# Kernel optimization log

Measured on AMD Instinct MI355X. Metric: run time of the kernel, lower is better.

## Reference

```python
import jax, jax.numpy as jnp
import numpy as np

PATCHES = 196
HEADS = 12


def build_attention_mask(patches, memory_tokens_list, extension=False):
    """Additive mask: masked entries -inf, allowed entries 0. Shape (1, Sq, Skv)."""
    class_tokens = len(memory_tokens_list) + 1
    input_tokens = patches + class_tokens
    total_tokens = input_tokens + sum(memory_tokens_list)
    mask = np.zeros((1, input_tokens, total_tokens), dtype=np.float32)
    mask[:, :, patches + 1:] = -np.inf
    prev = 0
    for i, mtok in enumerate(memory_tokens_list):
        ct = patches + 1 + i
        ms = input_tokens + prev
        me = ms + mtok
        if extension:
            mask[:, ct:, ct] = 0.0
            mask[:, ct:, ms:me] = 0.0
        else:
            mask[:, ct, ct] = 0.0
            mask[:, ct, ms:me] = 0.0
        prev += mtok
    return mask


def setup_inputs() -> dict:
    key = jax.random.key(0)
    ks = jax.random.split(key, 5)
    B, Sq, D, M = 64, PATCHES + 2, 768, 8  # 1 base class token + 1 memory class token
    std = 0.02
    return {
        "hidden_states": jax.random.normal(ks[0], (B, Sq, D), jnp.float32),
        "memory": jax.random.normal(ks[1], (1, M, D), jnp.float32) * std,
        "Wq": jax.random.normal(ks[2], (D, D), jnp.float32) * std,
        "bq": jnp.zeros((D,), jnp.float32),
        "Wk": jax.random.normal(ks[3], (D, D), jnp.float32) * std,
        "bk": jnp.zeros((D,), jnp.float32),
        "Wv": jax.random.normal(ks[4], (D, D), jnp.float32) * std,
        "bv": jnp.zeros((D,), jnp.float32),
    }


def _split_heads(x, heads):
    B, S, D = x.shape
    return x.reshape(B, S, heads, D // heads)  # bshd


def reference(hidden_states, memory, Wq, bq, Wk, bk, Wv, bv):
    B, Sq, D = hidden_states.shape
    M = memory.shape[1]
    head_dim = D // HEADS
    scale = 1.0 / jnp.sqrt(jnp.asarray(head_dim, hidden_states.dtype))
    # static additive mask (1, Sq, Skv)
    mask = jnp.asarray(build_attention_mask(PATCHES, [M]))

    with_memory = jnp.concatenate(
        [hidden_states, jnp.broadcast_to(memory, (B, M, D))], axis=1)  # (B, Skv, D)

    q = _split_heads(hidden_states @ Wq + bq, HEADS)  # (B,Sq,H,dh)
    k = _split_heads(with_memory @ Wk + bk, HEADS)    # (B,Skv,H,dh)
    v = _split_heads(with_memory @ Wv + bv, HEADS)

    scores = jnp.einsum("bqhd,bkhd->bhqk", q, k) * scale + mask[:, None]  # (B,H,Sq,Skv)
    probs = jax.nn.softmax(scores, axis=-1)  # dropout is identity in eval
    ctx = jnp.einsum("bhqk,bkhd->bqhd", probs, v)
    return ctx.reshape(B, Sq, D)
```

## Files before the change

### kernel.cpp

```cpp
#include <hip/hip_runtime.h>

typedef __attribute__((ext_vector_type(8))) short bf16x8;
typedef __attribute__((ext_vector_type(4))) float f32x4;
typedef __attribute__((ext_vector_type(4))) unsigned int u32x4;

#define NB 64
#define SQ 198
#define SKV 206
#define DM 768
#define NH 12
#define NROWS (NB * SKV)
#define NCOL 2304

static __device__ __forceinline__ unsigned short f2b(float f) {
  union { float f; unsigned u; } v; v.f = f;
  unsigned r = v.u + 0x7FFFu + ((v.u >> 16) & 1u);
  return (unsigned short)(r >> 16);
}

typedef const __attribute__((address_space(1))) unsigned int g_u32;
typedef __attribute__((address_space(3))) unsigned int l_u32;
static __device__ __forceinline__ void gload_lds16(const void* g, void* l) {
  __builtin_amdgcn_global_load_lds((g_u32*)g, (l_u32*)l, 16, 0, 0);
}

__global__ __launch_bounds__(256) void k_conv_x(const float* __restrict__ hid,
                                                const float* __restrict__ mem,
                                                unsigned short* __restrict__ xkv) {
  int idx = (blockIdx.x * 256 + threadIdx.x) * 8;
  int r = idx / DM;
  int c = idx - r * DM;
  int b = r / SKV, s = r - b * SKV;
  const float* src = (s < SQ) ? (hid + (b * SQ + s) * DM + c)
                              : (mem + (s - SQ) * DM + c);
  float4 v0 = ((const float4*)src)[0];
  float4 v1 = ((const float4*)src)[1];
  unsigned w0 = f2b(v0.x) | ((unsigned)f2b(v0.y) << 16);
  unsigned w1 = f2b(v0.z) | ((unsigned)f2b(v0.w) << 16);
  unsigned w2 = f2b(v1.x) | ((unsigned)f2b(v1.y) << 16);
  unsigned w3 = f2b(v1.z) | ((unsigned)f2b(v1.w) << 16);
  u32x4 o = {w0, w1, w2, w3};
  *(u32x4*)(xkv + idx) = o;
}

__global__ __launch_bounds__(256) void k_conv_w(const float* __restrict__ Wq,
                                                const float* __restrict__ Wk,
                                                const float* __restrict__ Wv,
                                                unsigned short* __restrict__ wt) {
  __shared__ float L[64][65];
  int w = blockIdx.z;
  int n0 = blockIdx.x * 64, k0 = blockIdx.y * 64;
  const float* W = (w == 0) ? Wq : (w == 1) ? Wk : Wv;
  int tid = threadIdx.x;
#pragma unroll
  for (int i = 0; i < 16; ++i) {
    int idx = i * 256 + tid;
    int lr = idx >> 6, lc = idx & 63;
    L[lr][lc] = W[(k0 + lr) * DM + n0 + lc];
  }
  __syncthreads();
  unsigned short* dst = wt + w * DM * DM;
#pragma unroll
  for (int o = 0; o < 2; ++o) {
    int gi = o * 256 + tid;
    int rn = gi >> 3, g = gi & 7;
    unsigned wrd[4];
#pragma unroll
    for (int jj = 0; jj < 4; ++jj) {
      float f0 = L[g * 8 + jj * 2 + 0][rn];
      float f1 = L[g * 8 + jj * 2 + 1][rn];
      wrd[jj] = f2b(f0) | ((unsigned)f2b(f1) << 16);
    }
    u32x4 o4 = {wrd[0], wrd[1], wrd[2], wrd[3]};
    *(u32x4*)(dst + (n0 + rn) * DM + k0 + g * 8) = o4;
  }
}

__global__ __launch_bounds__(512, 2) void k_gemm(const unsigned short* __restrict__ xkv,
                                                 const unsigned short* __restrict__ wt,
                                                 const float* __restrict__ bq,
                                                 const float* __restrict__ bk,
                                                 const float* __restrict__ bv,
                                                 unsigned short* __restrict__ cout) {
  __shared__ __align__(16) unsigned char smem[131072];
  int o = blockIdx.x, xcd = o & 7, rest = o >> 3;
  int sid = (xcd < 4 ? xcd * 59 : 236 + (xcd - 4) * 58) + rest;
  int mtile = sid / 9, ntile = sid - mtile * 9;
  int row0 = mtile * 256, col0 = ntile * 256;
  int w = ntile / 3;
  int colw0 = (ntile - w * 3) * 256;
  int tid = threadIdx.x, lane = tid & 63, wid = tid >> 6;
  int wm = wid >> 2, wn = wid & 3;
  int l = lane & 15, gq = lane >> 4;
  const unsigned short* wbase = wt + w * DM * DM;

  int sr = tid >> 2, pg = tid & 3, sg = pg ^ (sr & 3);
  int arow0 = row0 + sr;        if (arow0 > NROWS - 1) arow0 = NROWS - 1;
  int arow1 = row0 + 128 + sr;  if (arow1 > NROWS - 1) arow1 = NROWS - 1;
  const unsigned short* aP0 = xkv + arow0 * DM + sg * 8;
  const unsigned short* aP1 = xkv + arow1 * DM + sg * 8;
  const unsigned short* bP0 = wbase + (colw0 + sr) * DM + sg * 8;
  const unsigned short* bP1 = wbase + (colw0 + 128 + sr) * DM + sg * 8;
  int ldsW = wid * 1024;

  f32x4 zero = {0.f, 0.f, 0.f, 0.f};
  f32x4 acc[8][4];
#pragma unroll
  for (int i = 0; i < 8; ++i)
#pragma unroll
    for (int j = 0; j < 4; ++j) acc[i][j] = zero;

#pragma unroll
  for (int p = 0; p < 3; ++p) {
    gload_lds16(aP0 + p * 32, smem + p * 16384 + ldsW);
    gload_lds16(aP1 + p * 32, smem + p * 16384 + 8192 + ldsW);
    gload_lds16(bP0 + p * 32, smem + 65536 + p * 16384 + ldsW);
    gload_lds16(bP1 + p * 32, smem + 65536 + p * 16384 + 8192 + ldsW);
  }

  int swx = (gq * 16) ^ ((l & 3) << 4);
  int aRd = (wm * 128 + l) * 64 + swx;
  int bRd = 65536 + (wn * 64 + l) * 64 + swx;

  auto doTile = [&](int t) {
    int bo = (t & 3) * 16384;
    bf16x8 a[8], b[4];
#pragma unroll
    for (int mi = 0; mi < 8; ++mi) a[mi] = *(const bf16x8*)(smem + bo + aRd + mi * 1024);
#pragma unroll
    for (int ni = 0; ni < 4; ++ni) b[ni] = *(const bf16x8*)(smem + bo + bRd + ni * 1024);
    __builtin_amdgcn_s_setprio(1);
#pragma unroll
    for (int mi = 0; mi < 8; ++mi)
#pragma unroll
      for (int ni = 0; ni < 4; ++ni)
        acc[mi][ni] = __builtin_amdgcn_mfma_f32_16x16x32_bf16(a[mi], b[ni], acc[mi][ni], 0, 0, 0);
    __builtin_amdgcn_s_setprio(0);
  };

#pragma unroll 1
  for (int t = 0; t < 22; ++t) {
    asm volatile("s_waitcnt vmcnt(8)" ::: "memory");
    __builtin_amdgcn_s_barrier();
    asm volatile("" ::: "memory");
    if (t < 21) {
      int io = ((t + 3) & 3) * 16384;
      int kI = (t + 3) * 32;
      gload_lds16(aP0 + kI, smem + io + ldsW);
      gload_lds16(aP1 + kI, smem + io + 8192 + ldsW);
      gload_lds16(bP0 + kI, smem + 65536 + io + ldsW);
      gload_lds16(bP1 + kI, smem + 65536 + io + 8192 + ldsW);
    }
    doTile(t);
  }
  asm volatile("s_waitcnt vmcnt(4)" ::: "memory");
  __builtin_amdgcn_s_barrier();
  asm volatile("" ::: "memory");
  doTile(22);
  asm volatile("s_waitcnt vmcnt(0)" ::: "memory");
  __builtin_amdgcn_s_barrier();
  asm volatile("" ::: "memory");
  doTile(23);

  const float* bias = (w == 0) ? bq : (w == 1) ? bk : bv;
  float bb[4];
#pragma unroll
  for (int ni = 0; ni < 4; ++ni) bb[ni] = bias[colw0 + wn * 64 + ni * 16 + l];

  __syncthreads();
#pragma unroll
  for (int mi = 0; mi < 8; ++mi)
#pragma unroll
    for (int ni = 0; ni < 4; ++ni)
#pragma unroll
      for (int rr = 0; rr < 4; ++rr) {
        int row = wm * 128 + mi * 16 + gq * 4 + rr;
        int col = wn * 64 + ni * 16 + l;
        *(unsigned short*)(smem + row * 512 + ((col * 2) ^ ((row & 7) << 4))) =
            f2b(acc[mi][ni][rr] + bb[ni]);
      }
  __syncthreads();
#pragma unroll
  for (int it = 0; it < 16; ++it) {
    int gi = it * 512 + tid;
    int row = gi >> 5, gran = gi & 31;
    if (row0 + row < NROWS) {
      u32x4 v = *(const u32x4*)(smem + row * 512 + ((gran * 16) ^ ((row & 7) << 4)));
      *(u32x4*)(cout + (row0 + row) * NCOL + col0 + gran * 8) = v;
    }
  }
}

static __device__ __forceinline__ int vt_off(int row, int col) {
  return row * 416 + ((col * 2) ^ (((row >> 3) & 1) << 4));
}

__global__ __launch_bounds__(256, 3) void k_attn(const unsigned short* __restrict__ cqkv,
                                                 float* __restrict__ out) {
  __shared__ __align__(16) unsigned short Ksh[208 * 64];
  __shared__ __align__(16) unsigned char  VtB[64 * 416];
  int bh = blockIdx.x;
  int b = bh / NH, h = bh - b * NH;
  int tid = threadIdx.x, lane = tid & 63, wid = tid >> 6;
  int g = lane >> 4, l = lane & 15;
  const unsigned short* Cb = cqkv + (b * SKV) * NCOL + h * 64;

  if (tid < 64) *(unsigned*)(VtB + vt_off(tid, 206)) = 0u;
  for (int i = tid; i < 208 * 8; i += 256) {
    int row = i >> 3, gg = i & 7;
    int srow = (row < SKV) ? row : (SKV - 1);
    u32x4 v = *(const u32x4*)(Cb + srow * NCOL + 768 + gg * 8);
    *(u32x4*)((unsigned char*)Ksh + ((row * 128 + gg * 16) ^ ((row & 7) << 4))) = v;
  }
  for (int i = tid; i < 206 * 8; i += 256) {
    int key = i >> 3, gg = i & 7;
    u32x4 v = *(const u32x4*)(Cb + key * NCOL + 1536 + gg * 8);
    union { u32x4 v4; unsigned short e[8]; } u; u.v4 = v;
#pragma unroll
    for (int j = 0; j < 8; ++j)
      *(unsigned short*)(VtB + vt_off(gg * 8 + j, key)) = u.e[j];
  }
  __syncthreads();

  const float scale = 0.125f;
  f32x4 zero4 = {0.f, 0.f, 0.f, 0.f};
  int srcA = ((g & 1) << 5) + l;
  int srcB = srcA + 16;
  bool hiHalf = (g >= 2);

  for (int qt = wid; qt < 13; qt += 4) {
    int qr = qt * 16 + l;
    int qld = qr > 197 ? 197 : qr;
    const unsigned short* qp = Cb + qld * NCOL + g * 8;
    bf16x8 qa0 = *(const bf16x8*)qp;
    bf16x8 qa1 = *(const bf16x8*)(qp + 32);

    f32x4 sc[13];
#pragma unroll
    for (int nt = 0; nt < 13; ++nt) sc[nt] = zero4;
#pragma unroll
    for (int nt = 0; nt < 13; ++nt) {
      int key = nt * 16 + l;
      int rb = key * 128, sw = (key & 7) << 4, kb = g * 16;
      bf16x8 kb0 = *(const bf16x8*)((const unsigned char*)Ksh + rb + (kb ^ sw));
      bf16x8 kb1 = *(const bf16x8*)((const unsigned char*)Ksh + rb + ((kb + 64) ^ sw));
      sc[nt] = __builtin_amdgcn_mfma_f32_16x16x32_bf16(kb0, qa0, sc[nt], 0, 0, 0);
      sc[nt] = __builtin_amdgcn_mfma_f32_16x16x32_bf16(kb1, qa1, sc[nt], 0, 0, 0);
    }

    float mx = -1e30f;
#pragma unroll
    for (int nt = 0; nt < 13; ++nt)
#pragma unroll
      for (int r = 0; r < 4; ++r) {
        int key = nt * 16 + g * 4 + r;
        float s = sc[nt][r] * scale;
        bool ok = (key < 197 || qr == 197) && (key < SKV);
        s = ok ? s : -1e30f;
        sc[nt][r] = s;
        mx = fmaxf(mx, s);
      }
    mx = fmaxf(mx, __shfl_xor(mx, 16));
    mx = fmaxf(mx, __shfl_xor(mx, 32));
    float sum = 0.f;
#pragma unroll
    for (int nt = 0; nt < 13; ++nt)
#pragma unroll
      for (int r = 0; r < 4; ++r) {
        float p = __expf(sc[nt][r] - mx);
        sc[nt][r] = p;
        sum += p;
      }
    sum += __shfl_xor(sum, 16);
    sum += __shfl_xor(sum, 32);
    float inv = 1.0f / sum;

    unsigned pk0[13], pk1[13];
#pragma unroll
    for (int nt = 0; nt < 13; ++nt) {
      asm("v_cvt_pk_bf16_f32 %0, %1, %2" : "=v"(pk0[nt]) : "v"(sc[nt][0]), "v"(sc[nt][1]));
      asm("v_cvt_pk_bf16_f32 %0, %1, %2" : "=v"(pk1[nt]) : "v"(sc[nt][2]), "v"(sc[nt][3]));
    }

    f32x4 ctx[4];
#pragma unroll
    for (int dt = 0; dt < 4; ++dt) ctx[dt] = zero4;
#pragma unroll
    for (int c = 0; c < 7; ++c) {
      union { unsigned w[4]; bf16x8 v; } pa;
      if (c < 6) {
        int n0 = 2 * c, n1 = 2 * c + 1;
        unsigned a0 = (unsigned)__shfl((int)pk0[n0], srcA), b0 = (unsigned)__shfl((int)pk0[n1], srcA);
        unsigned a1 = (unsigned)__shfl((int)pk1[n0], srcA), b1 = (unsigned)__shfl((int)pk1[n1], srcA);
        unsigned a2 = (unsigned)__shfl((int)pk0[n0], srcB), b2 = (unsigned)__shfl((int)pk0[n1], srcB);
        unsigned a3 = (unsigned)__shfl((int)pk1[n0], srcB), b3 = (unsigned)__shfl((int)pk1[n1], srcB);
        pa.w[0] = hiHalf ? b0 : a0;
        pa.w[1] = hiHalf ? b1 : a1;
        pa.w[2] = hiHalf ? b2 : a2;
        pa.w[3] = hiHalf ? b3 : a3;
      } else {
        unsigned a0 = (unsigned)__shfl((int)pk0[12], srcA);
        unsigned a1 = (unsigned)__shfl((int)pk1[12], srcA);
        unsigned a2 = (unsigned)__shfl((int)pk0[12], srcB);
        unsigned a3 = (unsigned)__shfl((int)pk1[12], srcB);
        pa.w[0] = hiHalf ? 0u : a0;
        pa.w[1] = hiHalf ? 0u : a1;
        pa.w[2] = hiHalf ? 0u : a2;
        pa.w[3] = hiHalf ? 0u : a3;
      }
      int colb = c * 32 + g * 8;
      if (c == 6 && hiHalf) colb = 0;
#pragma unroll
      for (int dt = 0; dt < 4; ++dt) {
        bf16x8 vb = *(const bf16x8*)(VtB + vt_off(dt * 16 + l, colb));
        ctx[dt] = __builtin_amdgcn_mfma_f32_16x16x32_bf16(pa.v, vb, ctx[dt], 0, 0, 0);
      }
    }

    float invr[4];
#pragma unroll
    for (int r = 0; r < 4; ++r) invr[r] = __shfl(inv, g * 4 + r);
#pragma unroll
    for (int dt = 0; dt < 4; ++dt)
#pragma unroll
      for (int r = 0; r < 4; ++r) {
        int qo = qt * 16 + g * 4 + r;
        if (qo < SQ)
          out[(b * SQ + qo) * DM + h * 64 + dt * 16 + l] = ctx[dt][r] * invr[r];
      }
  }
}

extern "C" void kernel_launch(void* const* d_in, const int* in_sizes, int n_in,
                              void* d_out, int out_size, void* d_ws, size_t ws_size,
                              hipStream_t stream) {
  const float* hid = (const float*)d_in[0];
  const float* mem = (const float*)d_in[1];
  const float* Wq  = (const float*)d_in[2];
  const float* bq  = (const float*)d_in[3];
  const float* Wk  = (const float*)d_in[4];
  const float* bk  = (const float*)d_in[5];
  const float* Wv  = (const float*)d_in[6];
  const float* bv  = (const float*)d_in[7];
  float* out = (float*)d_out;

  unsigned short* xkv  = (unsigned short*)d_ws;
  unsigned short* wt   = xkv + NROWS * DM;
  unsigned short* cbuf = wt + 3 * DM * DM;

  k_conv_x<<<dim3(NROWS * DM / 8 / 256), 256, 0, stream>>>(hid, mem, xkv);
  k_conv_w<<<dim3(12, 12, 3), 256, 0, stream>>>(Wq, Wk, Wv, wt);
  k_gemm<<<dim3(468), 512, 0, stream>>>(xkv, wt, bq, bk, bv, cbuf);
  k_attn<<<dim3(NB * NH), 256, 0, stream>>>(cbuf, out);
}
```

Measured before the change: 105.0 us.

## Split GEMM K-tile into two MFMA phases with interleaved loads and new LDS swizzle

Restructures the QKV projection GEMM main loop so each K-tile is processed in two halves. LDS fragment reads, global-to-LDS prefetches and MFMA bursts are interleaved, separated by barriers and sched_barrier fences, in a ping-pong style schedule. It also changes the LDS XOR swizzle to use bits 1-2 of the row, aiming to reduce bank conflicts on 16-byte fragment reads. The extra barriers per tile add synchronisation overhead, and the hand-placed vmcnt waits must stay consistent with the prefetch depth.

```diff
diff --git a/kernel.cpp b/kernel.cpp
--- a/kernel.cpp
+++ b/kernel.cpp
@@ -94,13 +94,19 @@
   int l = lane & 15, gq = lane >> 4;
   const unsigned short* wbase = wt + w * DM * DM;
 
-  int sr = tid >> 2, pg = tid & 3, sg = pg ^ (sr & 3);
-  int arow0 = row0 + sr;        if (arow0 > NROWS - 1) arow0 = NROWS - 1;
-  int arow1 = row0 + 128 + sr;  if (arow1 > NROWS - 1) arow1 = NROWS - 1;
-  const unsigned short* aP0 = xkv + arow0 * DM + sg * 8;
-  const unsigned short* aP1 = xkv + arow1 * DM + sg * 8;
-  const unsigned short* bP0 = wbase + (colw0 + sr) * DM + sg * 8;
-  const unsigned short* bP1 = wbase + (colw0 + 128 + sr) * DM + sg * 8;
+  const unsigned short* aP0;
+  const unsigned short* aP1;
+  const unsigned short* bP0;
+  const unsigned short* bP1;
+  {
+    int sr = tid >> 2, pg = tid & 3, sg = pg ^ ((sr >> 1) & 3);
+    int ar0 = row0 + sr;       if (ar0 > NROWS - 1) ar0 = NROWS - 1;
+    int ar1 = row0 + 128 + sr; if (ar1 > NROWS - 1) ar1 = NROWS - 1;
+    aP0 = xkv + ar0 * DM + sg * 8;
+    aP1 = xkv + ar1 * DM + sg * 8;
+    bP0 = wbase + (colw0 + sr) * DM + sg * 8;
+    bP1 = wbase + (colw0 + 128 + sr) * DM + sg * 8;
+  }
   int ldsW = wid * 1024;
 
   f32x4 zero = {0.f, 0.f, 0.f, 0.f};
@@ -117,50 +123,62 @@
     gload_lds16(bP0 + p * 32, smem + 65536 + p * 16384 + ldsW);
     gload_lds16(bP1 + p * 32, smem + 65536 + p * 16384 + 8192 + ldsW);
   }
-
-  int swx = (gq * 16) ^ ((l & 3) << 4);
+  asm volatile("s_waitcnt vmcnt(8)" ::: "memory");
+  __builtin_amdgcn_s_barrier();
+
+  int swx = (gq * 16) ^ (((l >> 1) & 3) << 4);
   int aRd = (wm * 128 + l) * 64 + swx;
-  int bRd = 65536 + (wn * 64 + l) * 64 + swx;
-
-  auto doTile = [&](int t) {
-    int bo = (t & 3) * 16384;
-    bf16x8 a[8], b[4];
-#pragma unroll
-    for (int mi = 0; mi < 8; ++mi) a[mi] = *(const bf16x8*)(smem + bo + aRd + mi * 1024);
-#pragma unroll
-    for (int ni = 0; ni < 4; ++ni) b[ni] = *(const bf16x8*)(smem + bo + bRd + ni * 1024);
-    __builtin_amdgcn_s_setprio(1);
-#pragma unroll
-    for (int mi = 0; mi < 8; ++mi)
-#pragma unroll
-      for (int ni = 0; ni < 4; ++ni)
-        acc[mi][ni] = __builtin_amdgcn_mfma_f32_16x16x32_bf16(a[mi], b[ni], acc[mi][ni], 0, 0, 0);
-    __builtin_amdgcn_s_setprio(0);
-  };
+  int bRd = (wn * 64 + l) * 64 + swx;
 
 #pragma unroll 1
-  for (int t = 0; t < 22; ++t) {
-    asm volatile("s_waitcnt vmcnt(8)" ::: "memory");
-    __builtin_amdgcn_s_barrier();
-    asm volatile("" ::: "memory");
-    if (t < 21) {
-      int io = ((t + 3) & 3) * 16384;
-      int kI = (t + 3) * 32;
+  for (int t = 0; t < 24; ++t) {
+    int boA = (t & 3) * 16384;
+    int boB = 65536 + boA;
+    int io = ((t + 3) & 3) * 16384;
+    int kI = (t + 3) * 32;
+    bool st = (t < 21);
+    bf16x8 af[4], bfr[4];
+#pragma unroll
+    for (int mi = 0; mi < 4; ++mi) af[mi] = *(const bf16x8*)(smem + boA + aRd + mi * 1024);
+#pragma unroll
+    for (int ni = 0; ni < 4; ++ni) bfr[ni] = *(const bf16x8*)(smem + boB + bRd + ni * 1024);
+    if (st) {
       gload_lds16(aP0 + kI, smem + io + ldsW);
       gload_lds16(aP1 + kI, smem + io + 8192 + ldsW);
+    }
+    __builtin_amdgcn_s_barrier();
+    asm volatile("s_waitcnt lgkmcnt(0)" ::: "memory");
+    __builtin_amdgcn_sched_barrier(0);
+    __builtin_amdgcn_s_setprio(1);
+#pragma unroll
+    for (int mi = 0; mi < 4; ++mi)
+#pragma unroll
+      for (int ni = 0; ni < 4; ++ni)
+        acc[mi][ni] = __builtin_amdgcn_mfma_f32_16x16x32_bf16(af[mi], bfr[ni], acc[mi][ni], 0, 0, 0);
+    __builtin_amdgcn_s_setprio(0);
+    __builtin_amdgcn_s_barrier();
+    bf16x8 ag[4];
+#pragma unroll
+    for (int mi = 0; mi < 4; ++mi) ag[mi] = *(const bf16x8*)(smem + boA + aRd + (4 + mi) * 1024);
+    if (st) {
       gload_lds16(bP0 + kI, smem + 65536 + io + ldsW);
       gload_lds16(bP1 + kI, smem + 65536 + io + 8192 + ldsW);
     }
-    doTile(t);
-  }
-  asm volatile("s_waitcnt vmcnt(4)" ::: "memory");
-  __builtin_amdgcn_s_barrier();
-  asm volatile("" ::: "memory");
-  doTile(22);
-  asm volatile("s_waitcnt vmcnt(0)" ::: "memory");
-  __builtin_amdgcn_s_barrier();
-  asm volatile("" ::: "memory");
-  doTile(23);
+    __builtin_amdgcn_s_barrier();
+    asm volatile("s_waitcnt lgkmcnt(0)" ::: "memory");
+    __builtin_amdgcn_sched_barrier(0);
+    __builtin_amdgcn_s_setprio(1);
+#pragma unroll
+    for (int mi = 0; mi < 4; ++mi)
+#pragma unroll
+      for (int ni = 0; ni < 4; ++ni)
+        acc[4 + mi][ni] = __builtin_amdgcn_mfma_f32_16x16x32_bf16(ag[mi], bfr[ni], acc[4 + mi][ni], 0, 0, 0);
+    __builtin_amdgcn_s_setprio(0);
+    if (t < 21)       { asm volatile("s_waitcnt vmcnt(8)" ::: "memory"); }
+    else if (t == 21) { asm volatile("s_waitcnt vmcnt(4)" ::: "memory"); }
+    else if (t == 22) { asm volatile("s_waitcnt vmcnt(0)" ::: "memory"); }
+    __builtin_amdgcn_s_barrier();
+  }
 
   const float* bias = (w == 0) ? bq : (w == 1) ? bk : bv;
   float bb[4];
```

Result: no change. 104.6 us (-0.4%).
